# Performance work log

Hardware: AMD Instinct MI355X
Metric: run time of the kernel (lower is better)

The kernel has to match this reference:

```python
import jax, jax.numpy as jnp
from jax import lax
import numpy as np

HPDF = np.array([-0.0544158422, 0.3128715909, -0.6756307363, 0.5853546837,
                 0.0158291053, -0.284015543, -0.0004724846, 0.1287474266,
                 0.017369301, -0.0440882539, -0.0139810279, 0.008746094,
                 0.004870353, -0.0003917404, -0.0006754494, -0.0001174768],
                dtype=np.float32)


def setup_inputs() -> dict:
    key = jax.random.key(0)
    x = jax.random.normal(key, (8, 3, 512, 512), dtype=jnp.float32)
    hpdf = jnp.asarray(HPDF)
    return {"x": x, "hpdf": hpdf}


def _dwconv(inp, k2d, channels):
    # depthwise valid cross-correlation (matches F.conv2d with groups=C)
    n = k2d.shape[0]
    k = jnp.broadcast_to(k2d[None, None], (channels, 1, n, n))
    return lax.conv_general_dilated(
        inp, k, window_strides=(1, 1), padding='VALID',
        dimension_numbers=('NCHW', 'OIHW', 'NCHW'),
        feature_group_count=channels)


def reference(x, hpdf):
    B, C, H, W = x.shape
    n = hpdf.shape[0]  # 16 taps
    sign = (-1.0) ** jnp.arange(n, dtype=jnp.float32)
    lpdf = sign * hpdf[::-1]
    filters = [jnp.outer(lpdf, hpdf),   # LH
               jnp.outer(hpdf, lpdf),   # HL
               jnp.outer(hpdf, hpdf)]   # HH
    pad = n - 1  # 15
    xp = jnp.pad(x, ((0, 0), (0, 0), (pad, pad), (pad, pad)), mode='reflect')

    xis = []
    for f in filters:
        R = _dwconv(xp, f, C)                       # [B,C,H+15,W+15]
        xi = _dwconv(jnp.abs(R), jnp.abs(f[::-1, ::-1]), C)  # [B,C,H,W]
        # filter side length 16 is even -> roll by 1 on both spatial dims
        xi = jnp.roll(jnp.roll(xi, 1, axis=-1), 1, axis=-2)
        xis.append(xi)

    xi_stack = jnp.stack(xis, axis=0)               # [3,B,C,H,W]
    # p = -1: rho = (sum xi^p)^(-1/p) = sum(1/xi)
    rho = jnp.sum(1.0 / xi_stack, axis=0)
    wet = 1e10
    rho = jnp.minimum(rho, wet)
    rho = jnp.where(jnp.isnan(rho), wet, rho)
    mn = rho.min(axis=(-2, -1), keepdims=True)
    mx = rho.max(axis=(-2, -1), keepdims=True)
    rho = (rho - mn) / (mx - mn + 1e-8)
    score = jax.nn.sigmoid(1.0 - rho)
    return x * score
```

## Files before the change

kernel.cpp:

```cpp
#include <hip/hip_runtime.h>
#include <math.h>

#define IMG   512
#define NIMG  24
#define XST   72
#define TST   104
#define RST   56
#define UST   88
#define UOFF  4480
#define P1SZ  7296
#define TSZ   (48 * TST)

typedef _Float16 v8h __attribute__((ext_vector_type(8)));
typedef float    v4f __attribute__((ext_vector_type(4)));

__device__ __forceinline__ v8h load8(const _Float16* p) {
    union { uint4 u; v8h h; } c;
    c.u = *(const uint4*)p;
    return c.h;
}

__device__ __forceinline__ unsigned pkrtz(float a, float b) {
    union { __fp16 __attribute__((ext_vector_type(2))) v; unsigned u; } c;
    c.v = __builtin_amdgcn_cvt_pkrtz(a, b);
    return c.u;
}

__device__ __forceinline__ void store4(_Float16* p, v4f a) {
    union { _Float16 h[4]; uint2 u; } c;
    c.h[0] = (_Float16)a[0]; c.h[1] = (_Float16)a[1];
    c.h[2] = (_Float16)a[2]; c.h[3] = (_Float16)a[3];
    *(uint2*)p = c.u;
}

__device__ __forceinline__ void store4abs(_Float16* p, v4f a) {
    union { _Float16 h[4]; uint2 u; } c;
    c.h[0] = (_Float16)fabsf(a[0]); c.h[1] = (_Float16)fabsf(a[1]);
    c.h[2] = (_Float16)fabsf(a[2]); c.h[3] = (_Float16)fabsf(a[3]);
    *(uint2*)p = c.u;
}

__device__ __forceinline__ unsigned short f2bf(float f) {
    unsigned b = __float_as_uint(f);
    b = (b + 0x7fffu + ((b >> 16) & 1u)) >> 16;
    return (unsigned short)b;
}

__device__ __forceinline__ int refl(int g) {
    return g < 0 ? -g : (g >= IMG ? 2 * IMG - 2 - g : g);
}

__global__ __launch_bounds__(512, 6) void stego_stage1(
    const float* __restrict__ x, const float* __restrict__ hpdf,
    unsigned short* __restrict__ rho_out, float2* __restrict__ bmm)
{
    __shared__ __align__(16) _Float16 pool1[P1SZ];
    __shared__ __align__(16) _Float16 sTL[TSZ];
    __shared__ __align__(16) _Float16 sTH[TSZ];
    __shared__ __align__(16) _Float16 btab[512];
    __shared__ float red[16];

    const int tid = threadIdx.x;
    const int lane = tid & 63;
    const int wid = __builtin_amdgcn_readfirstlane(tid >> 6);
    const int n16 = lane & 15, quad = lane >> 4;

    const int blk = blockIdx.x;
    const int xcd = blk & 7;
    const int grp = blk >> 3;
    const int img = xcd + ((grp >> 7) << 3);
    const int tl  = grp & 127;
    const int Oi = (tl >> 4) << 6;
    const int Oj = (tl & 15) << 5;
    const float* ximg = x + (size_t)img * (IMG * IMG);

    {
        const int mode = tid >> 7, t = tid & 127;
        float v = 0.f;
        if (t >= 16 && t < 32) {
            int tap = t - 16;
            int idx = (mode == 0 || mode == 2) ? tap : 15 - tap;
            float c = hpdf[idx];
            if (mode == 1 && (tap & 1)) c = -c;
            if (mode >= 2) c = fabsf(c);
            v = c;
        }
        btab[tid] = (_Float16)v;
    }

    {
        const int cg = tid & 15, row0 = tid >> 4;
        const int c0 = Oj - 16 + 4 * cg;
        _Float16* dst = pool1 + row0 * XST + 4 * cg;
        if (Oi >= 15 && Oi <= 433 && Oj >= 16 && Oj <= 464) {
            const float* src = ximg + (size_t)(Oi - 15 + row0) * IMG + c0;
            #pragma unroll
            for (int k = 0; k < 3; ++k) {
                const int row = row0 + (k << 5);
                uint2 pv = make_uint2(0u, 0u);
                if (row < 94) {
                    float4 xv = *(const float4*)(src + (size_t)(k << 5) * IMG);
                    pv.x = pkrtz(xv.x, xv.y);
                    pv.y = pkrtz(xv.z, xv.w);
                }
                *(uint2*)(dst + (size_t)(k << 5) * XST) = pv;
            }
        } else {
            const int gj0 = refl(c0),     gj1 = refl(c0 + 1);
            const int gj2 = refl(c0 + 2), gj3 = refl(c0 + 3);
            #pragma unroll
            for (int k = 0; k < 3; ++k) {
                const int row = row0 + (k << 5);
                uint2 pv = make_uint2(0u, 0u);
                if (row < 94) {
                    const float* rsrc = ximg + (size_t)refl(Oi - 15 + row) * IMG;
                    pv.x = pkrtz(rsrc[gj0], rsrc[gj1]);
                    pv.y = pkrtz(rsrc[gj2], rsrc[gj3]);
                }
                *(uint2*)(dst + (size_t)(k << 5) * XST) = pv;
            }
        }
    }
    __syncthreads();

    v8h band[4], bandA[2];
    {
        const int boff  = 16 + quad * 8 - n16;
        const int boffA = 15 + quad * 8 - n16;
        #pragma unroll
        for (int m = 0; m < 4; ++m)
            #pragma unroll
            for (int j = 0; j < 8; ++j)
                band[m][j] = btab[m * 128 + boff + j];
        #pragma unroll
        for (int m = 0; m < 2; ++m)
            #pragma unroll
            for (int j = 0; j < 8; ++j)
                bandA[m][j] = btab[m * 128 + boffA + j];
    }

    for (int u = wid; u < 18; u += 8) {
        int mt = u % 6, nt = u / 6;
        int m0 = mt * 16, n0 = nt * 16;
        v8h a = load8(pool1 + (m0 + n16) * XST + n0 + quad * 8);
        v4f z = {0.f, 0.f, 0.f, 0.f};
        v4f cL = __builtin_amdgcn_mfma_f32_16x16x32_f16(a, bandA[1], z, 0, 0, 0);
        v4f cH = __builtin_amdgcn_mfma_f32_16x16x32_f16(a, bandA[0], z, 0, 0, 0);
        int off = (n0 + n16) * TST + m0 + quad * 4;
        store4(sTL + off, cL);
        store4(sTH + off, cH);
    }
    __syncthreads();

    float rho[4] = {0.f, 0.f, 0.f, 0.f};
    _Float16* Rb = pool1;
    _Float16* Ub = pool1 + UOFF;

    const int fB[3] = {0, 1, 0};
    const int fC[3] = {2, 3, 3};
    const int fD[3] = {3, 2, 3};

    #pragma unroll
    for (int f = 0; f < 3; ++f) {
        const _Float16* Tsrc = (f == 0) ? sTL : sTH;

        for (int u = wid; u < 15; u += 8) {
            int nt = u % 5, mt = u / 5;
            int i0 = nt * 16, c0 = mt * 16;
            v8h a = load8(Tsrc + (c0 + n16) * TST + i0 + quad * 8);
            v4f z = {0.f, 0.f, 0.f, 0.f};
            v4f acc = __builtin_amdgcn_mfma_f32_16x16x32_f16(a, band[fB[f]], z, 0, 0, 0);
            store4abs(Rb + (i0 + n16) * RST + c0 + quad * 4, acc);
        }
        __syncthreads();

        for (int u = wid; u < 10; u += 8) {
            int mt = u % 5, nt = u / 5;
            int i0 = mt * 16, j0 = nt * 16;
            v8h a = load8(Rb + (i0 + n16) * RST + j0 + quad * 8);
            v4f z = {0.f, 0.f, 0.f, 0.f};
            v4f acc = __builtin_amdgcn_mfma_f32_16x16x32_f16(a, band[fC[f]], z, 0, 0, 0);
            store4(Ub + (j0 + n16) * UST + i0 + quad * 4, acc);
        }
        __syncthreads();

        {
            int i0 = (wid & 3) * 16, c0 = (wid >> 2) * 16;
            v8h a = load8(Ub + (c0 + n16) * UST + i0 + quad * 8);
            v4f z = {0.f, 0.f, 0.f, 0.f};
            v4f acc = __builtin_amdgcn_mfma_f32_16x16x32_f16(a, band[fD[f]], z, 0, 0, 0);
            #pragma unroll
            for (int r = 0; r < 4; ++r) rho[r] += __builtin_amdgcn_rcpf(acc[r]);
        }
    }

    const size_t rbase = (size_t)img * (IMG * IMG);
    const int i_nat = Oi + (wid & 3) * 16 + n16;
    const int jb = Oj + ((wid >> 2) << 4) + quad * 4;
    float lmin = 1e38f, lmax = 0.f;
    unsigned pk0, pk1;
    {
        unsigned short b[4];
        #pragma unroll
        for (int r = 0; r < 4; ++r) {
            float v = rho[r];
            v = isnan(v) ? 1e10f : fminf(v, 1e10f);
            b[r] = f2bf(v);
            float rq = __uint_as_float((unsigned)b[r] << 16);
            lmin = fminf(lmin, rq);
            lmax = fmaxf(lmax, rq);
        }
        pk0 = (unsigned)b[0] | ((unsigned)b[1] << 16);
        pk1 = (unsigned)b[2] | ((unsigned)b[3] << 16);
    }
    *(uint2*)(rho_out + rbase + ((size_t)i_nat << 9) + jb) = make_uint2(pk0, pk1);

    #pragma unroll
    for (int off = 32; off >= 1; off >>= 1) {
        lmin = fminf(lmin, __shfl_xor(lmin, off));
        lmax = fmaxf(lmax, __shfl_xor(lmax, off));
    }
    if ((tid & 63) == 0) { red[wid] = lmin; red[8 + wid] = lmax; }
    __syncthreads();
    if (tid == 0) {
        float m0 = red[0], m1 = red[8];
        #pragma unroll
        for (int k = 1; k < 8; ++k) { m0 = fminf(m0, red[k]); m1 = fmaxf(m1, red[8 + k]); }
        bmm[(img << 7) + tl] = make_float2(m0, m1);
    }
}

__global__ __launch_bounds__(256) void stego_stage2(
    const float* __restrict__ x, const unsigned short* __restrict__ rho,
    const float2* __restrict__ bmm, float* __restrict__ out)
{
    __shared__ float sred[8];
    const int tid = threadIdx.x;
    const int lane = tid & 63;

    const int blk = blockIdx.x;
    const int xcd = blk & 7, grp = blk >> 3;
    const int img = xcd + ((grp >> 7) << 3);
    const int chunk = grp & 127;
    const int t = (img << 15) + (chunk << 8) + tid;

    float lmn = 1e38f, lmx = 0.f;
    if (tid < 128) { float2 p = bmm[(img << 7) + tid]; lmn = p.x; lmx = p.y; }
    #pragma unroll
    for (int off = 32; off >= 1; off >>= 1) {
        lmn = fminf(lmn, __shfl_xor(lmn, off));
        lmx = fmaxf(lmx, __shfl_xor(lmx, off));
    }
    if (tid < 128 && (tid & 63) == 0) { sred[tid >> 6] = lmn; sred[4 + (tid >> 6)] = lmx; }
    __syncthreads();
    const float mn = fminf(sred[0], sred[1]);
    const float mx = fmaxf(sred[4], sred[5]);
    const float inv = __builtin_amdgcn_rcpf(mx - mn + 1e-8f);

    const int i = (t >> 6) & 511;
    const int rrow = (i - 1) & 511;
    const size_t rb_off = ((size_t)img << 18) + ((size_t)rrow << 9) + ((size_t)lane << 3);
    uint4 rb = *(const uint4*)(rho + rb_off);
    unsigned ru[4] = {rb.x, rb.y, rb.z, rb.w};
    float f7 = __uint_as_float(ru[3] & 0xffff0000u);
    float r[8];
    r[0] = __shfl(f7, (lane + 63) & 63);
    r[1] = __uint_as_float(ru[0] << 16);
    r[2] = __uint_as_float(ru[0] & 0xffff0000u);
    r[3] = __uint_as_float(ru[1] << 16);
    r[4] = __uint_as_float(ru[1] & 0xffff0000u);
    r[5] = __uint_as_float(ru[2] << 16);
    r[6] = __uint_as_float(ru[2] & 0xffff0000u);
    r[7] = __uint_as_float(ru[3] << 16);

    const size_t base = (size_t)t << 3;
    const float* xrow = x + base;
    float4 xa = *(const float4*)xrow;
    float4 xb = *(const float4*)(xrow + 4);
    float xs[8] = {xa.x, xa.y, xa.z, xa.w, xb.x, xb.y, xb.z, xb.w};
    float os[8];
    #pragma unroll
    for (int k = 0; k < 8; ++k) {
        float rn = (r[k] - mn) * inv;
        os[k] = xs[k] * __builtin_amdgcn_rcpf(1.f + __expf(rn - 1.f));
    }
    float* orow = out + base;
    *(float4*)orow       = make_float4(os[0], os[1], os[2], os[3]);
    *(float4*)(orow + 4) = make_float4(os[4], os[5], os[6], os[7]);
}

extern "C" void kernel_launch(void* const* d_in, const int* in_sizes, int n_in,
                              void* d_out, int out_size, void* d_ws, size_t ws_size,
                              hipStream_t stream) {
    const float* x    = (const float*)d_in[0];
    const float* hpdf = (const float*)d_in[1];
    float* out = (float*)d_out;

    unsigned short* rho = (unsigned short*)d_ws;
    float2* bmm = (float2*)((char*)d_ws + (size_t)NIMG * IMG * IMG * 2);

    hipLaunchKernelGGL(stego_stage1, dim3(NIMG * 128), dim3(512), 0, stream,
                       x, hpdf, rho, bmm);
    hipLaunchKernelGGL(stego_stage2, dim3(NIMG * 128), dim3(256), 0, stream,
                       x, rho, bmm, out);
}
```

Baseline: 117.7 us.

## Batch three filter passes per stage to cut barriers; vectorize band loads

Shared memory is reorganized into one pool with separate R and U buffers per filter, so the R, U and final stages each run all three filters before a single barrier. This replaces six barriers with two. The band table is laid out as pre-shifted 8-element rows so each band fragment is fetched with one 16-byte LDS load instead of eight scalar reads. The cost is a larger LDS footprint, which could lower blocks per CU.

```diff
diff --git a/kernel.cpp b/kernel.cpp
--- a/kernel.cpp
+++ b/kernel.cpp
@@ -7,9 +7,16 @@
 #define TST   104
 #define RST   56
 #define UST   88
-#define UOFF  4480
-#define P1SZ  7296
-#define TSZ   (48 * TST)
+
+#define SA_TL  0
+#define SA_TH  4992
+#define SA_X   9984
+#define SA_R   9984
+#define RSZ    4480
+#define SA_U   0
+#define USZ    2816
+#define SA_FT  22112
+#define POOLSZ 23424
 
 typedef _Float16 v8h __attribute__((ext_vector_type(8)));
 typedef float    v4f __attribute__((ext_vector_type(4)));
@@ -54,10 +61,7 @@
     const float* __restrict__ x, const float* __restrict__ hpdf,
     unsigned short* __restrict__ rho_out, float2* __restrict__ bmm)
 {
-    __shared__ __align__(16) _Float16 pool1[P1SZ];
-    __shared__ __align__(16) _Float16 sTL[TSZ];
-    __shared__ __align__(16) _Float16 sTH[TSZ];
-    __shared__ __align__(16) _Float16 btab[512];
+    __shared__ __align__(16) _Float16 pool[POOLSZ];
     __shared__ float red[16];
 
     const int tid = threadIdx.x;
@@ -74,24 +78,25 @@
     const int Oj = (tl & 15) << 5;
     const float* ximg = x + (size_t)img * (IMG * IMG);
 
-    {
-        const int mode = tid >> 7, t = tid & 127;
+    for (int e = tid; e < 1312; e += 512) {
+        const int mode = e >> 3 == 0 ? 0 : (e / 328);
+        const int rem  = e - mode * 328;
+        const int tap  = (rem >> 3) + (rem & 7) - 16;
         float v = 0.f;
-        if (t >= 16 && t < 32) {
-            int tap = t - 16;
+        if (tap >= 0 && tap <= 15) {
             int idx = (mode == 0 || mode == 2) ? tap : 15 - tap;
             float c = hpdf[idx];
             if (mode == 1 && (tap & 1)) c = -c;
             if (mode >= 2) c = fabsf(c);
             v = c;
         }
-        btab[tid] = (_Float16)v;
+        pool[SA_FT + e] = (_Float16)v;
     }
 
     {
         const int cg = tid & 15, row0 = tid >> 4;
         const int c0 = Oj - 16 + 4 * cg;
-        _Float16* dst = pool1 + row0 * XST + 4 * cg;
+        _Float16* dst = pool + SA_X + row0 * XST + 4 * cg;
         if (Oi >= 15 && Oi <= 433 && Oj >= 16 && Oj <= 464) {
             const float* src = ximg + (size_t)(Oi - 15 + row0) * IMG + c0;
             #pragma unroll
@@ -125,68 +130,69 @@
 
     v8h band[4], bandA[2];
     {
-        const int boff  = 16 + quad * 8 - n16;
-        const int boffA = 15 + quad * 8 - n16;
+        const int sA = 16 + quad * 8 - n16;
         #pragma unroll
         for (int m = 0; m < 4; ++m)
-            #pragma unroll
-            for (int j = 0; j < 8; ++j)
-                band[m][j] = btab[m * 128 + boff + j];
+            band[m] = load8(pool + SA_FT + (m * 41 + sA) * 8);
         #pragma unroll
         for (int m = 0; m < 2; ++m)
-            #pragma unroll
-            for (int j = 0; j < 8; ++j)
-                bandA[m][j] = btab[m * 128 + boffA + j];
+            bandA[m] = load8(pool + SA_FT + (m * 41 + sA - 1) * 8);
     }
 
     for (int u = wid; u < 18; u += 8) {
         int mt = u % 6, nt = u / 6;
         int m0 = mt * 16, n0 = nt * 16;
-        v8h a = load8(pool1 + (m0 + n16) * XST + n0 + quad * 8);
+        v8h a = load8(pool + SA_X + (m0 + n16) * XST + n0 + quad * 8);
         v4f z = {0.f, 0.f, 0.f, 0.f};
         v4f cL = __builtin_amdgcn_mfma_f32_16x16x32_f16(a, bandA[1], z, 0, 0, 0);
         v4f cH = __builtin_amdgcn_mfma_f32_16x16x32_f16(a, bandA[0], z, 0, 0, 0);
         int off = (n0 + n16) * TST + m0 + quad * 4;
-        store4(sTL + off, cL);
-        store4(sTH + off, cH);
+        store4(pool + SA_TL + off, cL);
+        store4(pool + SA_TH + off, cH);
     }
     __syncthreads();
 
     float rho[4] = {0.f, 0.f, 0.f, 0.f};
-    _Float16* Rb = pool1;
-    _Float16* Ub = pool1 + UOFF;
-
     const int fB[3] = {0, 1, 0};
     const int fC[3] = {2, 3, 3};
     const int fD[3] = {3, 2, 3};
 
     #pragma unroll
     for (int f = 0; f < 3; ++f) {
-        const _Float16* Tsrc = (f == 0) ? sTL : sTH;
-
+        const _Float16* Tsrc = pool + (f == 0 ? SA_TL : SA_TH);
+        _Float16* Rf = pool + SA_R + f * RSZ;
         for (int u = wid; u < 15; u += 8) {
             int nt = u % 5, mt = u / 5;
             int i0 = nt * 16, c0 = mt * 16;
             v8h a = load8(Tsrc + (c0 + n16) * TST + i0 + quad * 8);
             v4f z = {0.f, 0.f, 0.f, 0.f};
             v4f acc = __builtin_amdgcn_mfma_f32_16x16x32_f16(a, band[fB[f]], z, 0, 0, 0);
-            store4abs(Rb + (i0 + n16) * RST + c0 + quad * 4, acc);
-        }
-        __syncthreads();
-
+            store4abs(Rf + (i0 + n16) * RST + c0 + quad * 4, acc);
+        }
+    }
+    __syncthreads();
+
+    #pragma unroll
+    for (int f = 0; f < 3; ++f) {
+        const _Float16* Rf = pool + SA_R + f * RSZ;
+        _Float16* Uf = pool + SA_U + f * USZ;
         for (int u = wid; u < 10; u += 8) {
             int mt = u % 5, nt = u / 5;
             int i0 = mt * 16, j0 = nt * 16;
-            v8h a = load8(Rb + (i0 + n16) * RST + j0 + quad * 8);
+            v8h a = load8(Rf + (i0 + n16) * RST + j0 + quad * 8);
             v4f z = {0.f, 0.f, 0.f, 0.f};
             v4f acc = __builtin_amdgcn_mfma_f32_16x16x32_f16(a, band[fC[f]], z, 0, 0, 0);
-            store4(Ub + (j0 + n16) * UST + i0 + quad * 4, acc);
-        }
-        __syncthreads();
-
-        {
-            int i0 = (wid & 3) * 16, c0 = (wid >> 2) * 16;
-            v8h a = load8(Ub + (c0 + n16) * UST + i0 + quad * 8);
+            store4(Uf + (j0 + n16) * UST + i0 + quad * 4, acc);
+        }
+    }
+    __syncthreads();
+
+    {
+        const int i0 = (wid & 3) * 16, c0 = (wid >> 2) * 16;
+        #pragma unroll
+        for (int f = 0; f < 3; ++f) {
+            const _Float16* Uf = pool + SA_U + f * USZ;
+            v8h a = load8(Uf + (c0 + n16) * UST + i0 + quad * 8);
             v4f z = {0.f, 0.f, 0.f, 0.f};
             v4f acc = __builtin_amdgcn_mfma_f32_16x16x32_f16(a, band[fD[f]], z, 0, 0, 0);
             #pragma unroll
```

New measurement: 108.6 us. 7.8% less time.
